# Kernel optimization log

Measured on AMD Instinct MI355X. Metric: run time of the kernel, lower is better.

## Reference

```python
import jax, jax.numpy as jnp
import numpy as np

TAU = 2.0   # membrane decay time constant
TH = 1.0    # firing threshold

N, T, D = 64, 64, 8192


def setup_inputs() -> dict:
    key = jax.random.key(0)
    k1, k2, k3 = jax.random.split(key, 3)
    x = jax.random.normal(k1, (N, T, D), dtype=jnp.float32)
    momentum = jax.random.uniform(k2, (1,), dtype=jnp.float32)
    lamb = jax.random.uniform(k3, (1,), dtype=jnp.float32)
    return {"x": x, "momentum": momentum, "lamb": lamb}


def reference(x, momentum, lamb):
    """Momentum LIF neuron scanned over the time axis.

    Assumed dynamics (CUDA kernel source unavailable; reduces to standard
    STBP hard-reset LIF when momentum == 0 and lamb == 0):
        v_t = momentum * v_{t-1} + x_t - lamb * u_{t-1}   # momentum on input current
        u_t = (1 - 1/tau) * u_{t-1} + v_t                 # leaky integrate
        s_t = H(u_t - th)                                 # spike
        u_t = u_t * (1 - s_t)                             # hard reset
    x: [N, T, D] -> spikes: [N, T, D]
    """
    decay = 1.0 - 1.0 / TAU
    mom = momentum[0]
    lb = lamb[0]

    def step(carry, xt):
        u, v = carry                      # each [N, D]
        v = mom * v + xt - lb * u
        u = decay * u + v
        s = (u >= TH).astype(xt.dtype)
        u = u * (1.0 - s)                 # hard reset
        return (u, v), s

    xs = jnp.swapaxes(x, 0, 1)            # [T, N, D] for time scan
    u0 = jnp.zeros_like(x[:, 0])
    v0 = jnp.zeros_like(x[:, 0])
    _, spikes = jax.lax.scan(step, (u0, v0), xs)
    return jnp.swapaxes(spikes, 0, 1)      # [N, T, D]
```

## Files before the change

### kernel.cpp

```cpp
#include <hip/hip_runtime.h>
#include <stdint.h>


#define N_ 64
#define T_ 64
#define D_ 8192
#define PF 16

__global__ __launch_bounds__(256) void MomentumLIF_kernel(
    const float* __restrict__ x,
    const float* __restrict__ momp,
    const float* __restrict__ lambp,
    float* __restrict__ out)
{
#pragma clang fp contract(off)
    float mom  = momp[0];
    float lamb = lambp[0];
    const float decay = 0.5f;

    asm volatile("" : "+s"(mom), "+s"(lamb));

    const int tid = blockIdx.x * blockDim.x + threadIdx.x;
    const int n = tid >> 13;
    const int d = tid & (D_ - 1);

    const float* xp = x   + (size_t)n * T_ * D_ + d;
    float*       op = out + (size_t)n * T_ * D_ + d;

    float xs[PF];

#pragma unroll
    for (int i = 0; i < PF; ++i) {
        const float* a = xp + (size_t)i * D_;
        asm volatile("global_load_dword %0, %1, off" : "=v"(xs[i]) : "v"(a));
    }

    float u = 0.f, v = 0.f;
    uint32_t blo = 0u, bhi = 0u;

#pragma unroll
    for (int t = 0; t < T_ - PF; ++t) {
        const int slot = t & (PF - 1);
        asm volatile("s_waitcnt vmcnt(15)" : "+v"(xs[slot]));
        const float xt = xs[slot];
        const float* a = xp + (size_t)(t + PF) * D_;
        asm volatile("global_load_dword %0, %1, off" : "=v"(xs[slot]) : "v"(a));

        float t1 = mom * v;
        float t2 = lamb * u;
        v = (t1 + xt) - t2;
        u = decay * u + v;
        const bool sp = (u >= 1.0f);
        if (t < 32) blo |= ((uint32_t)sp) << t;
        else        bhi |= ((uint32_t)sp) << (t - 32);
        u = sp ? 0.0f : u;
    }

    asm volatile("s_waitcnt vmcnt(0)"
                 : "+v"(xs[0]),  "+v"(xs[1]),  "+v"(xs[2]),  "+v"(xs[3]),
                   "+v"(xs[4]),  "+v"(xs[5]),  "+v"(xs[6]),  "+v"(xs[7]),
                   "+v"(xs[8]),  "+v"(xs[9]),  "+v"(xs[10]), "+v"(xs[11]),
                   "+v"(xs[12]), "+v"(xs[13]), "+v"(xs[14]), "+v"(xs[15]));

#pragma unroll
    for (int t = T_ - PF; t < T_; ++t) {
        const float xt = xs[t & (PF - 1)];
        float t1 = mom * v;
        float t2 = lamb * u;
        v = (t1 + xt) - t2;
        u = decay * u + v;
        const bool sp = (u >= 1.0f);
        if (t < 32) blo |= ((uint32_t)sp) << t;
        else        bhi |= ((uint32_t)sp) << (t - 32);
        u = sp ? 0.0f : u;
    }

#pragma unroll
    for (int t = 0; t < T_; ++t) {
        const uint32_t bit = ((t < 32 ? blo : bhi) >> (t & 31)) & 1u;
        op[(size_t)t * D_] = bit ? 1.0f : 0.0f;
    }
}

extern "C" void kernel_launch(void* const* d_in, const int* in_sizes, int n_in,
                              void* d_out, int out_size, void* d_ws, size_t ws_size,
                              hipStream_t stream) {
    const float* x    = (const float*)d_in[0];
    const float* momp = (const float*)d_in[1];
    const float* lamb = (const float*)d_in[2];
    float* out = (float*)d_out;

    const int threads = N_ * D_;
    dim3 block(256);
    dim3 grid(threads / 256);
    hipLaunchKernelGGL(MomentumLIF_kernel, grid, block, 0, stream,
                       x, momp, lamb, out);
}
```

Before: 234.6 us.

## Split into bit-packed compute kernel and vectorized nontemporal spike-expansion kernel

The scan kernel now writes only a packed 64-bit spike mask per chain to workspace, and a second kernel expands the masks into the float output using 16-byte nontemporal stores. The aim is to replace the strided scalar 4-byte output stores in the scan kernel with fully coalesced wide writes. The cost is an extra launch and a small workspace round trip, and the two phases are serialized. A leading s_waitcnt is also added before the prefetch loads.

```diff
diff --git a/kernel.cpp b/kernel.cpp
--- a/kernel.cpp
+++ b/kernel.cpp
@@ -7,11 +7,13 @@
 #define D_ 8192
 #define PF 16
 
-__global__ __launch_bounds__(256) void MomentumLIF_kernel(
+typedef __attribute__((ext_vector_type(4))) float f32x4;
+
+__global__ __launch_bounds__(256) void lif_compute_pack(
     const float* __restrict__ x,
     const float* __restrict__ momp,
     const float* __restrict__ lambp,
-    float* __restrict__ out)
+    uint2* __restrict__ ws)
 {
 #pragma clang fp contract(off)
     float mom  = momp[0];
@@ -23,12 +25,11 @@
     const int tid = blockIdx.x * blockDim.x + threadIdx.x;
     const int n = tid >> 13;
     const int d = tid & (D_ - 1);
+    const float* xp = x + (size_t)n * T_ * D_ + d;
 
-    const float* xp = x   + (size_t)n * T_ * D_ + d;
-    float*       op = out + (size_t)n * T_ * D_ + d;
+    asm volatile("s_waitcnt vmcnt(0)" ::: "memory");
 
     float xs[PF];
-
 #pragma unroll
     for (int i = 0; i < PF; ++i) {
         const float* a = xp + (size_t)i * D_;
@@ -75,11 +76,36 @@
         u = sp ? 0.0f : u;
     }
 
-#pragma unroll
-    for (int t = 0; t < T_; ++t) {
-        const uint32_t bit = ((t < 32 ? blo : bhi) >> (t & 31)) & 1u;
-        op[(size_t)t * D_] = bit ? 1.0f : 0.0f;
-    }
+    ws[tid] = make_uint2(blo, bhi);
+}
+
+__global__ __launch_bounds__(256) void lif_expand(
+    const uint2* __restrict__ ws,
+    float* __restrict__ out)
+{
+    const int g = blockIdx.x * blockDim.x + threadIdx.x;
+    const size_t e = (size_t)g << 2;
+    const int nt = (int)(e >> 13);
+    const int t  = nt & (T_ - 1);
+    const int n  = nt >> 6;
+    const int d  = (int)(e & (D_ - 1));
+    const int chain = (n << 13) + d;
+
+    const uint2 w0 = ws[chain + 0];
+    const uint2 w1 = ws[chain + 1];
+    const uint2 w2 = ws[chain + 2];
+    const uint2 w3 = ws[chain + 3];
+
+    const int  sh = t & 31;
+    const bool hi = (t >= 32);
+
+    f32x4 o;
+    o.x = (((hi ? w0.y : w0.x) >> sh) & 1u) ? 1.0f : 0.0f;
+    o.y = (((hi ? w1.y : w1.x) >> sh) & 1u) ? 1.0f : 0.0f;
+    o.z = (((hi ? w2.y : w2.x) >> sh) & 1u) ? 1.0f : 0.0f;
+    o.w = (((hi ? w3.y : w3.x) >> sh) & 1u) ? 1.0f : 0.0f;
+
+    __builtin_nontemporal_store(o, reinterpret_cast<f32x4*>(out) + g);
 }
 
 extern "C" void kernel_launch(void* const* d_in, const int* in_sizes, int n_in,
@@ -89,10 +115,17 @@
     const float* momp = (const float*)d_in[1];
     const float* lamb = (const float*)d_in[2];
     float* out = (float*)d_out;
+    uint2* ws  = (uint2*)d_ws;
 
-    const int threads = N_ * D_;
-    dim3 block(256);
-    dim3 grid(threads / 256);
-    hipLaunchKernelGGL(MomentumLIF_kernel, grid, block, 0, stream,
-                       x, momp, lamb, out);
+    {
+        dim3 block(256);
+        dim3 grid((N_ * D_) / 256);
+        hipLaunchKernelGGL(lif_compute_pack, grid, block, 0, stream,
+                           x, momp, lamb, ws);
+    }
+    {
+        dim3 block(256);
+        dim3 grid((N_ * T_ * D_ / 4) / 256);
+        hipLaunchKernelGGL(lif_expand, grid, block, 0, stream, ws, out);
+    }
 }
```

Result: no change. 231.0 us (-1.5%).
